# Kernel tuning notes

Measured on AMD Instinct MI355X. Metric: run time of the kernel, lower is better.

## Reference

```python
import jax, jax.numpy as jnp
import numpy as np

B, N, D = 32, 1024, 128


def setup_inputs() -> dict:
    key = jax.random.key(0)
    ks = jax.random.split(key, 8)
    scale = 0.05
    P = jax.random.normal(ks[0], (B, N, D), dtype=jnp.float32)
    w_itr_att = jax.random.normal(ks[1], (3 * D,), dtype=jnp.float32) * scale
    w1 = jax.random.normal(ks[2], (2 * D, D), dtype=jnp.float32) * scale
    w2 = jax.random.normal(ks[3], (2 * D, D), dtype=jnp.float32) * scale
    w3 = jax.random.normal(ks[4], (2 * D, D), dtype=jnp.float32) * scale
    b1 = jnp.zeros((D,), dtype=jnp.float32)
    b2 = jnp.zeros((D,), dtype=jnp.float32)
    b3 = jnp.zeros((D,), dtype=jnp.float32)
    return {"P": P, "w_itr_att": w_itr_att, "w1": w1, "w2": w2,
            "w3": w3, "b1": b1, "b2": b2, "b3": b3}


def reference(P, w_itr_att, w1, w2, w3, b1, b2, b3):
    # P: [b, n, d]
    d = P.shape[-1]
    # Original builds alphaP[b,i,:,j] = concat(P[b,j], P[b,i], P[b,j]*P[b,i])
    # and A[b,i,j] = w_itr_att . alphaP[b,i,:,j]. Decompose w to avoid the
    # O(n^2 * 3d) tensor while computing identical math.
    wa, wb, wc = w_itr_att[:d], w_itr_att[d:2 * d], w_itr_att[2 * d:]
    A = (P @ wb)[:, :, None] + (P @ wa)[:, None, :] \
        + jnp.einsum('bid,bjd->bij', P * wc, P)  # [b, n, n]
    SA = jax.nn.softmax(A, axis=-1)              # softmax over j (axis=2)
    itr_attn = jnp.einsum('bij,bjd->bid', SA, P)  # batch_dot(SA, P)
    # Fuse gate (dropout is identity at inference)
    P_concat = jnp.concatenate([P, itr_attn], axis=2)  # [b, n, 2d]
    z = jnp.tanh(P_concat @ w1 + b1)
    r = jax.nn.sigmoid(P_concat @ w2 + b2)
    f = jax.nn.sigmoid(P_concat @ w3 + b3)
    return r * P + f * z
```

## Files before the change

kernel.cpp:

```cpp
#include <hip/hip_runtime.h>
#include <math.h>

#define BB 32
#define NN 1024
#define DD 128

typedef __bf16 bf16;
typedef bf16 bf16x4 __attribute__((ext_vector_type(4)));
typedef bf16 bf16x8 __attribute__((ext_vector_type(8)));
typedef float f32x4 __attribute__((ext_vector_type(4)));
typedef float f32x16 __attribute__((ext_vector_type(16)));

#define MFMA16(a, b, c) __builtin_amdgcn_mfma_f32_16x16x32_bf16(a, b, c, 0, 0, 0)
#define MFMA32(a, b, c) __builtin_amdgcn_mfma_f32_32x32x16_bf16(a, b, c, 0, 0, 0)

__device__ inline bf16x4 swap32(bf16x4 v) {
    union { bf16x4 h; int i[2]; } u, r;
    u.h = v;
    r.i[0] = __shfl_xor(u.i[0], 32, 64);
    r.i[1] = __shfl_xor(u.i[1], 32, 64);
    return r.h;
}

#define LTS 133
__global__ __launch_bounds__(256) void k_prep(const float* __restrict__ P,
                                              const float* __restrict__ w_itr,
                                              bf16* __restrict__ Xbf,
                                              bf16* __restrict__ Pq,
                                              bf16* __restrict__ Ptp,
                                              float* __restrict__ t) {
    __shared__ float Lt[64 * LTS];
    int tid = threadIdx.x;
    int b = blockIdx.x >> 4, g = blockIdx.x & 15;
    int n0 = g * 64;
    long base = ((long)b * NN + n0) * DD;
#pragma unroll
    for (int i = 0; i < 8; ++i) {
        int idx = tid + i * 256;
        int row = idx >> 5, c4 = idx & 31;
        *(float4*)&Lt[row * LTS + c4 * 4] = *(const float4*)&P[base + row * 128 + c4 * 4];
    }
    __syncthreads();
    {
        int row = tid >> 2, q = tid & 3;
        float s = 0.f;
#pragma unroll
        for (int kk = 0; kk < 32; ++kk) {
            int k = 4 * kk + q;
            s += Lt[row * LTS + k] * w_itr[k];
        }
        s += __shfl_xor(s, 1);
        s += __shfl_xor(s, 2);
        if (q == 0) t[(long)b * NN + n0 + row] = s;
    }
    const float* wc = w_itr + 2 * DD;
#pragma unroll
    for (int i = 0; i < 4; ++i) {
        int idx = tid + i * 256;
        int row = idx >> 4, seg = idx & 15;
        float4 va = *(const float4*)&Lt[row * LTS + seg * 8];
        float4 vb = *(const float4*)&Lt[row * LTS + seg * 8 + 4];
        float4 wa4 = *(const float4*)&wc[seg * 8];
        float4 wb4 = *(const float4*)&wc[seg * 8 + 4];
        float fv[8] = {va.x, va.y, va.z, va.w, vb.x, vb.y, vb.z, vb.w};
        float wv[8] = {wa4.x, wa4.y, wa4.z, wa4.w, wb4.x, wb4.y, wb4.z, wb4.w};
        bf16x8 xv, qv;
#pragma unroll
        for (int e = 0; e < 8; ++e) {
            xv[e] = (bf16)fv[e];
            qv[e] = (bf16)(fv[e] * wv[e]);
        }
        long rowg = (long)b * NN + n0 + row;
        *(bf16x8*)&Xbf[rowg * 128 + seg * 8] = xv;
        *(bf16x8*)&Pq[rowg * 128 + seg * 8] = qv;
    }
#pragma unroll
    for (int i = 0; i < 4; ++i) {
        int idx = tid + i * 256;
        int d = idx >> 3, c = idx & 7;
        bf16x8 v;
#pragma unroll
        for (int e = 0; e < 8; ++e) v[e] = (bf16)Lt[(c * 8 + e) * LTS + d];
        *(bf16x8*)&Ptp[((long)b * DD + d) * NN + n0 + c * 8] = v;
    }
}

__global__ __launch_bounds__(256) void k_prepw(const float* __restrict__ w1,
                                               const float* __restrict__ w2,
                                               const float* __restrict__ w3,
                                               bf16* __restrict__ WtG) {
    __shared__ float Lw[32][33];
    int bi = blockIdx.x;
    int mat = bi >> 5, rem = bi & 31;
    int kt = rem >> 2, ct = rem & 3;
    const float* wsrc = (mat == 0) ? w1 : ((mat == 1) ? w2 : w3);
    int tid = threadIdx.x;
#pragma unroll
    for (int p = 0; p < 4; ++p) {
        int idx = tid + p * 256;
        int kr = idx >> 5, c = idx & 31;
        Lw[kr][c] = wsrc[(kt * 32 + kr) * DD + ct * 32 + c];
    }
    __syncthreads();
    int colg = tid >> 3, kq = tid & 7;
    bf16x4 v;
#pragma unroll
    for (int e = 0; e < 4; ++e) v[e] = (bf16)Lw[kq * 4 + e][colg];
    *(bf16x4*)&WtG[(mat * 128 + ct * 32 + colg) * 256 + kt * 32 + kq * 4] = v;
}

__global__ __launch_bounds__(256, 3) void k_attn(const bf16* __restrict__ Xbf,
                                                 const bf16* __restrict__ Pq,
                                                 const bf16* __restrict__ Ptp,
                                                 const float* __restrict__ t,
                                                 const bf16* __restrict__ WtG,
                                                 const float* __restrict__ b1,
                                                 const float* __restrict__ b2,
                                                 const float* __restrict__ b3,
                                                 float* __restrict__ out) {
    __shared__ __align__(16) char smem[51200];
    float* PA   = (float*)smem;
    bf16*  Wst  = (bf16*)smem;
    float* ost  = (float*)smem;
    bf16*  Xsh  = (bf16*)(smem + 33792);
    float* lbuf = (float*)(smem + 50688);

    const int tid = threadIdx.x;
    const int kh = tid >> 6, lane = tid & 63;
    const int col = lane & 31, q = lane >> 5;
    const int b = blockIdx.x & 31, qt = blockIdx.x >> 5;
    const long qrow0 = (long)b * NN + qt * 32;
    const long kvrow = (long)b * NN;

    bf16x8 Qb[8];
#pragma unroll
    for (int c = 0; c < 8; ++c)
        Qb[c] = *(const bf16x8*)&Pq[(qrow0 + col) * 128 + c * 16 + q * 8];

    f32x16 O[4];
#pragma unroll
    for (int mt = 0; mt < 4; ++mt)
#pragma unroll
        for (int r = 0; r < 16; ++r) O[mt][r] = 0.f;
    float lsum = 0.f;

    for (int kt = 0; kt < 8; ++kt) {
        int j0 = kh * 256 + kt * 32;
        bf16x8 kf[8];
#pragma unroll
        for (int c = 0; c < 8; ++c)
            kf[c] = *(const bf16x8*)&Xbf[(kvrow + j0 + col) * 128 + c * 16 + q * 8];
        bf16x8 vf[4][2];
#pragma unroll
        for (int mt = 0; mt < 4; ++mt)
#pragma unroll
            for (int kc = 0; kc < 2; ++kc)
                vf[mt][kc] = *(const bf16x8*)&Ptp[((long)b * DD + mt * 32 + col) * NN +
                                                  j0 + kc * 16 + q * 8];
        float tqs[16];
#pragma unroll
        for (int i = 0; i < 4; ++i) {
            float4 tv = *(const float4*)&t[kvrow + j0 + 8 * i + 4 * q];
            tqs[4 * i + 0] = tv.x; tqs[4 * i + 1] = tv.y;
            tqs[4 * i + 2] = tv.z; tqs[4 * i + 3] = tv.w;
        }
        f32x16 S;
#pragma unroll
        for (int r = 0; r < 16; ++r) S[r] = 0.f;
#pragma unroll
        for (int c = 0; c < 8; ++c) S = MFMA32(kf[c], Qb[c], S);

        float pv[16];
#pragma unroll
        for (int r = 0; r < 16; ++r) {
            float e = __expf(fminf(S[r] + tqs[r], 80.f));
            pv[r] = e;
            lsum += e;
        }
        bf16x4 Qd[4];
#pragma unroll
        for (int i = 0; i < 4; ++i)
#pragma unroll
            for (int e = 0; e < 4; ++e) Qd[i][e] = (bf16)pv[4 * i + e];
        bf16x4 sA = q ? Qd[0] : Qd[1];
        bf16x4 rA = swap32(sA);
        bf16x4 sB = q ? Qd[2] : Qd[3];
        bf16x4 rB = swap32(sB);
        bf16x4 lo0 = q ? rA : Qd[0], hi0 = q ? Qd[1] : rA;
        bf16x4 lo1 = q ? rB : Qd[2], hi1 = q ? Qd[3] : rB;
        bf16x8 f0, f1;
#pragma unroll
        for (int e = 0; e < 4; ++e) {
            f0[e] = lo0[e]; f0[4 + e] = hi0[e];
            f1[e] = lo1[e]; f1[4 + e] = hi1[e];
        }
#pragma unroll
        for (int mt = 0; mt < 4; ++mt) {
            O[mt] = MFMA32(vf[mt][0], f0, O[mt]);
            O[mt] = MFMA32(vf[mt][1], f1, O[mt]);
        }
    }

    float l2 = lsum + __shfl_xor(lsum, 32, 64);
    if (q == 0) lbuf[kh * 32 + col] = l2;
    if (kh & 1) {
        int slot = kh >> 1;
#pragma unroll
        for (int mt = 0; mt < 4; ++mt)
#pragma unroll
            for (int r = 0; r < 16; ++r) {
                int d = mt * 32 + (r & 3) + 8 * (r >> 2) + 4 * q;
                PA[slot * 4224 + d * 33 + col] = O[mt][r];
            }
    }
    __syncthreads();
    if (!(kh & 1)) {
        int slot = kh >> 1;
#pragma unroll
        for (int mt = 0; mt < 4; ++mt)
#pragma unroll
            for (int r = 0; r < 16; ++r) {
                int d = mt * 32 + (r & 3) + 8 * (r >> 2) + 4 * q;
                O[mt][r] += PA[slot * 4224 + d * 33 + col];
            }
    }
    __syncthreads();
    if (kh == 2) {
#pragma unroll
        for (int mt = 0; mt < 4; ++mt)
#pragma unroll
            for (int r = 0; r < 16; ++r) {
                int d = mt * 32 + (r & 3) + 8 * (r >> 2) + 4 * q;
                PA[d * 33 + col] = O[mt][r];
            }
    } else if (kh & 1) {
        int t128 = (kh >> 1) * 64 + lane;
#pragma unroll
        for (int i = 0; i < 4; ++i) {
            int idx = t128 + i * 128;
            int row = idx >> 4, seg = idx & 15;
            *(bf16x8*)&Xsh[row * 264 + seg * 8] =
                *(const bf16x8*)&Xbf[(qrow0 + row) * 128 + seg * 8];
        }
    }
    __syncthreads();
    if (kh == 0) {
        float ltot = lbuf[col] + lbuf[32 + col] + lbuf[64 + col] + lbuf[96 + col];
        float linv = 1.f / ltot;
#pragma unroll
        for (int mt = 0; mt < 4; ++mt)
#pragma unroll
            for (int r = 0; r < 16; ++r) {
                int d = mt * 32 + (r & 3) + 8 * (r >> 2) + 4 * q;
                float v = (O[mt][r] + PA[d * 33 + col]) * linv;
                Xsh[col * 264 + 128 + d] = (bf16)v;
            }
    }

    const int ln = lane & 15, q3 = lane >> 4;
    const int rh = kh & 1, ch = kh >> 1;
    f32x4 gz[4], gr[4];
    float rres[16];
#pragma unroll
    for (int mat = 0; mat < 3; ++mat) {
        f32x4 acc[4];
#pragma unroll
        for (int nt = 0; nt < 4; ++nt) acc[nt] = (f32x4){0.f, 0.f, 0.f, 0.f};
#pragma unroll
        for (int k2 = 0; k2 < 4; ++k2) {
            __syncthreads();
#pragma unroll
            for (int i = 0; i < 4; ++i) {
                int idx = tid + i * 256;
                *(float4*)&Wst[(idx >> 3) * 72 + (idx & 7) * 8] =
                    *(const float4*)&WtG[(mat * 128 + (idx >> 3)) * 256 + k2 * 64 +
                                         (idx & 7) * 8];
            }
            __syncthreads();
#pragma unroll
            for (int kc2 = 0; kc2 < 2; ++kc2) {
                bf16x8 Af = *(const bf16x8*)&Xsh[(rh * 16 + ln) * 264 + k2 * 64 +
                                                 kc2 * 32 + q3 * 8];
#pragma unroll
                for (int nt = 0; nt < 4; ++nt) {
                    bf16x8 Bf = *(const bf16x8*)&Wst[(ch * 64 + nt * 16 + ln) * 72 +
                                                     kc2 * 32 + q3 * 8];
                    acc[nt] = MFMA16(Af, Bf, acc[nt]);
                }
            }
        }
        const float* bp = (mat == 0) ? b1 : ((mat == 1) ? b2 : b3);
#pragma unroll
        for (int nt = 0; nt < 4; ++nt) {
            int colc = ch * 64 + nt * 16 + ln;
            float bb = bp[colc];
#pragma unroll
            for (int r = 0; r < 4; ++r) {
                float y = acc[nt][r] + bb;
                if (mat == 0) gz[nt][r] = tanhf(y);
                else if (mat == 1) gr[nt][r] = 1.f / (1.f + __expf(-y));
                else {
                    float fg = 1.f / (1.f + __expf(-y));
                    int lrow = rh * 16 + q3 * 4 + r;
                    float p = (float)Xsh[lrow * 264 + colc];
                    rres[nt * 4 + r] = gr[nt][r] * p + fg * gz[nt][r];
                }
            }
        }
    }
    __syncthreads();
#pragma unroll
    for (int nt = 0; nt < 4; ++nt)
#pragma unroll
        for (int r = 0; r < 4; ++r)
            ost[(rh * 16 + q3 * 4 + r) * 132 + ch * 64 + nt * 16 + ln] = rres[nt * 4 + r];
    __syncthreads();
#pragma unroll
    for (int i = 0; i < 4; ++i) {
        int idx = tid + i * 256;
        int row = idx >> 5, c4 = idx & 31;
        float4 v = *(const float4*)&ost[row * 132 + c4 * 4];
        *(float4*)&out[(qrow0 + row) * 128 + c4 * 4] = v;
    }
}

extern "C" void kernel_launch(void* const* d_in, const int* in_sizes, int n_in,
                              void* d_out, int out_size, void* d_ws, size_t ws_size,
                              hipStream_t stream) {
    const float* P     = (const float*)d_in[0];
    const float* w_itr = (const float*)d_in[1];
    const float* w1    = (const float*)d_in[2];
    const float* w2    = (const float*)d_in[3];
    const float* w3    = (const float*)d_in[4];
    const float* b1    = (const float*)d_in[5];
    const float* b2    = (const float*)d_in[6];
    const float* b3    = (const float*)d_in[7];
    float* out = (float*)d_out;

    char* wsb = (char*)d_ws;
    bf16* Xbf  = (bf16*)(wsb);
    bf16* Pq   = (bf16*)(wsb + 8388608);
    bf16* Ptp  = (bf16*)(wsb + 16777216);
    float* tws = (float*)(wsb + 25165824);
    bf16* WtG  = (bf16*)(wsb + 25296896);

    k_prep<<<dim3(BB * 16), dim3(256), 0, stream>>>(P, w_itr, Xbf, Pq, Ptp, tws);
    k_prepw<<<dim3(96), dim3(256), 0, stream>>>(w1, w2, w3, WtG);
    k_attn<<<dim3(1024), dim3(256), 0, stream>>>(Xbf, Pq, Ptp, tws, WtG, b1, b2, b3, out);
}
```

Baseline: 176.6 us.

## Switch attention to 16x16 MFMA with 2x2 query/key-split waves, merge prep kernels

The attention loop now uses 16x16x32 MFMAs. Each wave owns 16 query rows and half of the keys, replacing 32x32 tiles split four ways over keys. This shrinks the cross-wave reduction from four partial O tiles to two, cuts LDS use so more blocks fit, and drops the exp clamp. The weight-transpose kernel is folded into the prep kernel as extra blocks, and prep now uses 32-row tiles with register-based row loads, saving one launch. The trade-off is more shuffle work to rebuild the probability operand and twice the K/V fragment loads per query row, since each key tile is loaded by two waves.

```diff
diff --git a/kernel.cpp b/kernel.cpp
--- a/kernel.cpp
+++ b/kernel.cpp
@@ -9,104 +9,98 @@
 typedef bf16 bf16x4 __attribute__((ext_vector_type(4)));
 typedef bf16 bf16x8 __attribute__((ext_vector_type(8)));
 typedef float f32x4 __attribute__((ext_vector_type(4)));
-typedef float f32x16 __attribute__((ext_vector_type(16)));
 
 #define MFMA16(a, b, c) __builtin_amdgcn_mfma_f32_16x16x32_bf16(a, b, c, 0, 0, 0)
-#define MFMA32(a, b, c) __builtin_amdgcn_mfma_f32_32x32x16_bf16(a, b, c, 0, 0, 0)
-
-__device__ inline bf16x4 swap32(bf16x4 v) {
-    union { bf16x4 h; int i[2]; } u, r;
-    u.h = v;
-    r.i[0] = __shfl_xor(u.i[0], 32, 64);
-    r.i[1] = __shfl_xor(u.i[1], 32, 64);
-    return r.h;
-}
 
 #define LTS 133
 __global__ __launch_bounds__(256) void k_prep(const float* __restrict__ P,
                                               const float* __restrict__ w_itr,
+                                              const float* __restrict__ w1,
+                                              const float* __restrict__ w2,
+                                              const float* __restrict__ w3,
                                               bf16* __restrict__ Xbf,
                                               bf16* __restrict__ Pq,
                                               bf16* __restrict__ Ptp,
-                                              float* __restrict__ t) {
-    __shared__ float Lt[64 * LTS];
+                                              float* __restrict__ t,
+                                              bf16* __restrict__ WtG) {
+    __shared__ __align__(16) float Lt[32 * LTS];
     int tid = threadIdx.x;
-    int b = blockIdx.x >> 4, g = blockIdx.x & 15;
-    int n0 = g * 64;
-    long base = ((long)b * NN + n0) * DD;
-#pragma unroll
-    for (int i = 0; i < 8; ++i) {
+    if (blockIdx.x >= 1024) {
+        float (*Lw)[33] = (float(*)[33])Lt;
+        int bi = blockIdx.x - 1024;
+        int mat = bi >> 5, rem = bi & 31;
+        int kt = rem >> 2, ct = rem & 3;
+        const float* wsrc = (mat == 0) ? w1 : ((mat == 1) ? w2 : w3);
+#pragma unroll
+        for (int p = 0; p < 4; ++p) {
+            int idx = tid + p * 256;
+            Lw[idx >> 5][idx & 31] = wsrc[(kt * 32 + (idx >> 5)) * DD + ct * 32 + (idx & 31)];
+        }
+        __syncthreads();
+        int colg = tid >> 3, kq = tid & 7;
+        bf16x4 v;
+#pragma unroll
+        for (int e = 0; e < 4; ++e) v[e] = (bf16)Lw[kq * 4 + e][colg];
+        *(bf16x4*)&WtG[(mat * 128 + ct * 32 + colg) * 256 + kt * 32 + kq * 4] = v;
+        return;
+    }
+    int b = blockIdx.x >> 5, g = blockIdx.x & 31;
+    int n0 = g * 32;
+    int row = tid >> 3, q8 = tid & 7, d0 = q8 * 16;
+    long rowg = (long)b * NN + n0 + row;
+    float r[16];
+#pragma unroll
+    for (int i = 0; i < 4; ++i) {
+        float4 v = *(const float4*)&P[rowg * DD + d0 + 4 * i];
+        r[4 * i + 0] = v.x; r[4 * i + 1] = v.y; r[4 * i + 2] = v.z; r[4 * i + 3] = v.w;
+        *(float4*)&Lt[row * LTS + d0 + 4 * i] = v;
+    }
+    {
+        float wa[16];
+#pragma unroll
+        for (int i = 0; i < 4; ++i) {
+            float4 wv = *(const float4*)&w_itr[d0 + 4 * i];
+            wa[4 * i + 0] = wv.x; wa[4 * i + 1] = wv.y;
+            wa[4 * i + 2] = wv.z; wa[4 * i + 3] = wv.w;
+        }
+        float s = 0.f;
+#pragma unroll
+        for (int k = 0; k < 16; ++k) s += r[k] * wa[k];
+        s += __shfl_xor(s, 1); s += __shfl_xor(s, 2); s += __shfl_xor(s, 4);
+        if (q8 == 0) t[rowg] = s;
+    }
+    {
+        const float* wc = w_itr + 2 * DD;
+        float wcr[16];
+#pragma unroll
+        for (int i = 0; i < 4; ++i) {
+            float4 wv = *(const float4*)&wc[d0 + 4 * i];
+            wcr[4 * i + 0] = wv.x; wcr[4 * i + 1] = wv.y;
+            wcr[4 * i + 2] = wv.z; wcr[4 * i + 3] = wv.w;
+        }
+#pragma unroll
+        for (int h = 0; h < 2; ++h) {
+            bf16x8 xv, qv;
+#pragma unroll
+            for (int e = 0; e < 8; ++e) {
+                float f = r[8 * h + e];
+                xv[e] = (bf16)f;
+                qv[e] = (bf16)(f * wcr[8 * h + e]);
+            }
+            *(bf16x8*)&Xbf[rowg * DD + d0 + 8 * h] = xv;
+            *(bf16x8*)&Pq[rowg * DD + d0 + 8 * h] = qv;
+        }
+    }
+    __syncthreads();
+#pragma unroll
+    for (int i = 0; i < 2; ++i) {
         int idx = tid + i * 256;
-        int row = idx >> 5, c4 = idx & 31;
-        *(float4*)&Lt[row * LTS + c4 * 4] = *(const float4*)&P[base + row * 128 + c4 * 4];
-    }
-    __syncthreads();
-    {
-        int row = tid >> 2, q = tid & 3;
-        float s = 0.f;
-#pragma unroll
-        for (int kk = 0; kk < 32; ++kk) {
-            int k = 4 * kk + q;
-            s += Lt[row * LTS + k] * w_itr[k];
-        }
-        s += __shfl_xor(s, 1);
-        s += __shfl_xor(s, 2);
-        if (q == 0) t[(long)b * NN + n0 + row] = s;
-    }
-    const float* wc = w_itr + 2 * DD;
-#pragma unroll
-    for (int i = 0; i < 4; ++i) {
-        int idx = tid + i * 256;
-        int row = idx >> 4, seg = idx & 15;
-        float4 va = *(const float4*)&Lt[row * LTS + seg * 8];
-        float4 vb = *(const float4*)&Lt[row * LTS + seg * 8 + 4];
-        float4 wa4 = *(const float4*)&wc[seg * 8];
-        float4 wb4 = *(const float4*)&wc[seg * 8 + 4];
-        float fv[8] = {va.x, va.y, va.z, va.w, vb.x, vb.y, vb.z, vb.w};
-        float wv[8] = {wa4.x, wa4.y, wa4.z, wa4.w, wb4.x, wb4.y, wb4.z, wb4.w};
-        bf16x8 xv, qv;
-#pragma unroll
-        for (int e = 0; e < 8; ++e) {
-            xv[e] = (bf16)fv[e];
-            qv[e] = (bf16)(fv[e] * wv[e]);
-        }
-        long rowg = (long)b * NN + n0 + row;
-        *(bf16x8*)&Xbf[rowg * 128 + seg * 8] = xv;
-        *(bf16x8*)&Pq[rowg * 128 + seg * 8] = qv;
-    }
-#pragma unroll
-    for (int i = 0; i < 4; ++i) {
-        int idx = tid + i * 256;
-        int d = idx >> 3, c = idx & 7;
+        int d = idx >> 2, c = idx & 3;
         bf16x8 v;
 #pragma unroll
         for (int e = 0; e < 8; ++e) v[e] = (bf16)Lt[(c * 8 + e) * LTS + d];
         *(bf16x8*)&Ptp[((long)b * DD + d) * NN + n0 + c * 8] = v;
     }
-}
-
-__global__ __launch_bounds__(256) void k_prepw(const float* __restrict__ w1,
-                                               const float* __restrict__ w2,
-                                               const float* __restrict__ w3,
-                                               bf16* __restrict__ WtG) {
-    __shared__ float Lw[32][33];
-    int bi = blockIdx.x;
-    int mat = bi >> 5, rem = bi & 31;
-    int kt = rem >> 2, ct = rem & 3;
-    const float* wsrc = (mat == 0) ? w1 : ((mat == 1) ? w2 : w3);
-    int tid = threadIdx.x;
-#pragma unroll
-    for (int p = 0; p < 4; ++p) {
-        int idx = tid + p * 256;
-        int kr = idx >> 5, c = idx & 31;
-        Lw[kr][c] = wsrc[(kt * 32 + kr) * DD + ct * 32 + c];
-    }
-    __syncthreads();
-    int colg = tid >> 3, kq = tid & 7;
-    bf16x4 v;
-#pragma unroll
-    for (int e = 0; e < 4; ++e) v[e] = (bf16)Lw[kq * 4 + e][colg];
-    *(bf16x4*)&WtG[(mat * 128 + ct * 32 + colg) * 256 + kt * 32 + kq * 4] = v;
 }
 
 __global__ __launch_bounds__(256, 3) void k_attn(const bf16* __restrict__ Xbf,
@@ -118,147 +112,121 @@
                                                  const float* __restrict__ b2,
                                                  const float* __restrict__ b3,
                                                  float* __restrict__ out) {
-    __shared__ __align__(16) char smem[51200];
+    __shared__ __align__(16) char smem[35840];
     float* PA   = (float*)smem;
     bf16*  Wst  = (bf16*)smem;
     float* ost  = (float*)smem;
-    bf16*  Xsh  = (bf16*)(smem + 33792);
-    float* lbuf = (float*)(smem + 50688);
+    bf16*  Xsh  = (bf16*)(smem + 18432);
+    float* lbuf = (float*)(smem + 35328);
 
     const int tid = threadIdx.x;
-    const int kh = tid >> 6, lane = tid & 63;
-    const int col = lane & 31, q = lane >> 5;
+    const int w = tid >> 6, lane = tid & 63;
+    const int ln = lane & 15, qd = lane >> 4;
+    const int qsub = w & 1, kh = w >> 1;
     const int b = blockIdx.x & 31, qt = blockIdx.x >> 5;
     const long qrow0 = (long)b * NN + qt * 32;
     const long kvrow = (long)b * NN;
-
-    bf16x8 Qb[8];
-#pragma unroll
-    for (int c = 0; c < 8; ++c)
-        Qb[c] = *(const bf16x8*)&Pq[(qrow0 + col) * 128 + c * 16 + q * 8];
-
-    f32x16 O[4];
-#pragma unroll
-    for (int mt = 0; mt < 4; ++mt)
-#pragma unroll
-        for (int r = 0; r < 16; ++r) O[mt][r] = 0.f;
+    const long myq = qrow0 + qsub * 16;
+
+    bf16x8 Qb[4];
+#pragma unroll
+    for (int c = 0; c < 4; ++c)
+        Qb[c] = *(const bf16x8*)&Pq[(myq + ln) * DD + c * 32 + qd * 8];
+
+    f32x4 O[8];
+#pragma unroll
+    for (int dt = 0; dt < 8; ++dt) O[dt] = (f32x4){0.f, 0.f, 0.f, 0.f};
     float lsum = 0.f;
 
-    for (int kt = 0; kt < 8; ++kt) {
-        int j0 = kh * 256 + kt * 32;
-        bf16x8 kf[8];
-#pragma unroll
-        for (int c = 0; c < 8; ++c)
-            kf[c] = *(const bf16x8*)&Xbf[(kvrow + j0 + col) * 128 + c * 16 + q * 8];
-        bf16x8 vf[4][2];
-#pragma unroll
-        for (int mt = 0; mt < 4; ++mt)
-#pragma unroll
-            for (int kc = 0; kc < 2; ++kc)
-                vf[mt][kc] = *(const bf16x8*)&Ptp[((long)b * DD + mt * 32 + col) * NN +
-                                                  j0 + kc * 16 + q * 8];
-        float tqs[16];
+    for (int it = 0; it < 16; ++it) {
+        const int j0 = kh * 512 + it * 32;
+        bf16x8 kf0[4], kf1[4];
+#pragma unroll
+        for (int c = 0; c < 4; ++c) {
+            kf0[c] = *(const bf16x8*)&Xbf[(kvrow + j0 + ln) * DD + c * 32 + qd * 8];
+            kf1[c] = *(const bf16x8*)&Xbf[(kvrow + j0 + 16 + ln) * DD + c * 32 + qd * 8];
+        }
+        bf16x8 vf[8];
+#pragma unroll
+        for (int dt = 0; dt < 8; ++dt)
+            vf[dt] = *(const bf16x8*)&Ptp[((long)b * DD + dt * 16 + ln) * NN + j0 + qd * 8];
+        float4 tv0 = *(const float4*)&t[kvrow + j0 + 4 * qd];
+        float4 tv1 = *(const float4*)&t[kvrow + j0 + 16 + 4 * qd];
+
+        f32x4 S0 = (f32x4){0.f, 0.f, 0.f, 0.f}, S1 = S0;
+#pragma unroll
+        for (int c = 0; c < 4; ++c) S0 = MFMA16(kf0[c], Qb[c], S0);
+#pragma unroll
+        for (int c = 0; c < 4; ++c) S1 = MFMA16(kf1[c], Qb[c], S1);
+
+        float t0s[4] = {tv0.x, tv0.y, tv0.z, tv0.w};
+        float t1s[4] = {tv1.x, tv1.y, tv1.z, tv1.w};
+        bf16x4 a4, c4;
+#pragma unroll
+        for (int r = 0; r < 4; ++r) {
+            float e0 = __expf(S0[r] + t0s[r]);
+            float e1 = __expf(S1[r] + t1s[r]);
+            lsum += e0 + e1;
+            a4[r] = (bf16)e0;
+            c4[r] = (bf16)e1;
+        }
+        union { bf16x4 h; int i[2]; } ua, ub, s16, s32, s48, r16, r32, r48;
+        ua.h = a4; ub.h = c4;
+        s16.i[0] = (qd < 2) ? ua.i[0] : ub.i[0];
+        s16.i[1] = (qd < 2) ? ua.i[1] : ub.i[1];
+        r16.i[0] = __shfl_xor(s16.i[0], 16, 64);
+        r16.i[1] = __shfl_xor(s16.i[1], 16, 64);
+        s32.i[0] = (qd & 1) ? ua.i[0] : ub.i[0];
+        s32.i[1] = (qd & 1) ? ua.i[1] : ub.i[1];
+        r32.i[0] = __shfl_xor(s32.i[0], 32, 64);
+        r32.i[1] = __shfl_xor(s32.i[1], 32, 64);
+        s48.i[0] = (qd == 2) ? ua.i[0] : ub.i[0];
+        s48.i[1] = (qd == 2) ? ua.i[1] : ub.i[1];
+        r48.i[0] = __shfl_xor(s48.i[0], 48, 64);
+        r48.i[1] = __shfl_xor(s48.i[1], 48, 64);
+        union { bf16x8 h; int i[4]; } Bp;
+        int lo0 = (qd == 0) ? ua.i[0] : (qd == 1) ? r48.i[0] : (qd == 2) ? r32.i[0] : r16.i[0];
+        int lo1 = (qd == 0) ? ua.i[1] : (qd == 1) ? r48.i[1] : (qd == 2) ? r32.i[1] : r16.i[1];
+        int hi0 = (qd == 0) ? r16.i[0] : (qd == 1) ? r32.i[0] : (qd == 2) ? r48.i[0] : ub.i[0];
+        int hi1 = (qd == 0) ? r16.i[1] : (qd == 1) ? r32.i[1] : (qd == 2) ? r48.i[1] : ub.i[1];
+        Bp.i[0] = lo0; Bp.i[1] = lo1; Bp.i[2] = hi0; Bp.i[3] = hi1;
+#pragma unroll
+        for (int dt = 0; dt < 8; ++dt) O[dt] = MFMA16(vf[dt], Bp.h, O[dt]);
+    }
+
+    lsum += __shfl_xor(lsum, 16, 64);
+    lsum += __shfl_xor(lsum, 32, 64);
+    if (lane < 16) lbuf[kh * 32 + qsub * 16 + ln] = lsum;
+    if (kh == 1) {
+#pragma unroll
+        for (int dt = 0; dt < 8; ++dt)
+            *(f32x4*)&PA[(qsub * 16 + ln) * 132 + dt * 16 + qd * 4] = O[dt];
+    }
+    __syncthreads();
+    if (kh == 0) {
+        float ltot = lbuf[qsub * 16 + ln] + lbuf[32 + qsub * 16 + ln];
+        float linv = 1.f / ltot;
+#pragma unroll
+        for (int dt = 0; dt < 8; ++dt) {
+            f32x4 pa = *(const f32x4*)&PA[(qsub * 16 + ln) * 132 + dt * 16 + qd * 4];
+            bf16x4 o4;
+#pragma unroll
+            for (int r = 0; r < 4; ++r) o4[r] = (bf16)((O[dt][r] + pa[r]) * linv);
+            *(bf16x4*)&Xsh[(qsub * 16 + ln) * 264 + 128 + dt * 16 + qd * 4] = o4;
+        }
+    } else {
+        int tl = tid - 128;
 #pragma unroll
         for (int i = 0; i < 4; ++i) {
-            float4 tv = *(const float4*)&t[kvrow + j0 + 8 * i + 4 * q];
-            tqs[4 * i + 0] = tv.x; tqs[4 * i + 1] = tv.y;
-            tqs[4 * i + 2] = tv.z; tqs[4 * i + 3] = tv.w;
-        }
-        f32x16 S;
-#pragma unroll
-        for (int r = 0; r < 16; ++r) S[r] = 0.f;
-#pragma unroll
-        for (int c = 0; c < 8; ++c) S = MFMA32(kf[c], Qb[c], S);
-
-        float pv[16];
-#pragma unroll
-        for (int r = 0; r < 16; ++r) {
-            float e = __expf(fminf(S[r] + tqs[r], 80.f));
-            pv[r] = e;
-            lsum += e;
-        }
-        bf16x4 Qd[4];
-#pragma unroll
-        for (int i = 0; i < 4; ++i)
-#pragma unroll
-            for (int e = 0; e < 4; ++e) Qd[i][e] = (bf16)pv[4 * i + e];
-        bf16x4 sA = q ? Qd[0] : Qd[1];
-        bf16x4 rA = swap32(sA);
-        bf16x4 sB = q ? Qd[2] : Qd[3];
-        bf16x4 rB = swap32(sB);
-        bf16x4 lo0 = q ? rA : Qd[0], hi0 = q ? Qd[1] : rA;
-        bf16x4 lo1 = q ? rB : Qd[2], hi1 = q ? Qd[3] : rB;
-        bf16x8 f0, f1;
-#pragma unroll
-        for (int e = 0; e < 4; ++e) {
-            f0[e] = lo0[e]; f0[4 + e] = hi0[e];
-            f1[e] = lo1[e]; f1[4 + e] = hi1[e];
-        }
-#pragma unroll
-        for (int mt = 0; mt < 4; ++mt) {
-            O[mt] = MFMA32(vf[mt][0], f0, O[mt]);
-            O[mt] = MFMA32(vf[mt][1], f1, O[mt]);
-        }
-    }
-
-    float l2 = lsum + __shfl_xor(lsum, 32, 64);
-    if (q == 0) lbuf[kh * 32 + col] = l2;
-    if (kh & 1) {
-        int slot = kh >> 1;
-#pragma unroll
-        for (int mt = 0; mt < 4; ++mt)
-#pragma unroll
-            for (int r = 0; r < 16; ++r) {
-                int d = mt * 32 + (r & 3) + 8 * (r >> 2) + 4 * q;
-                PA[slot * 4224 + d * 33 + col] = O[mt][r];
-            }
-    }
-    __syncthreads();
-    if (!(kh & 1)) {
-        int slot = kh >> 1;
-#pragma unroll
-        for (int mt = 0; mt < 4; ++mt)
-#pragma unroll
-            for (int r = 0; r < 16; ++r) {
-                int d = mt * 32 + (r & 3) + 8 * (r >> 2) + 4 * q;
-                O[mt][r] += PA[slot * 4224 + d * 33 + col];
-            }
-    }
-    __syncthreads();
-    if (kh == 2) {
-#pragma unroll
-        for (int mt = 0; mt < 4; ++mt)
-#pragma unroll
-            for (int r = 0; r < 16; ++r) {
-                int d = mt * 32 + (r & 3) + 8 * (r >> 2) + 4 * q;
-                PA[d * 33 + col] = O[mt][r];
-            }
-    } else if (kh & 1) {
-        int t128 = (kh >> 1) * 64 + lane;
-#pragma unroll
-        for (int i = 0; i < 4; ++i) {
-            int idx = t128 + i * 128;
+            int idx = tl + i * 128;
             int row = idx >> 4, seg = idx & 15;
             *(bf16x8*)&Xsh[row * 264 + seg * 8] =
-                *(const bf16x8*)&Xbf[(qrow0 + row) * 128 + seg * 8];
-        }
-    }
-    __syncthreads();
-    if (kh == 0) {
-        float ltot = lbuf[col] + lbuf[32 + col] + lbuf[64 + col] + lbuf[96 + col];
-        float linv = 1.f / ltot;
-#pragma unroll
-        for (int mt = 0; mt < 4; ++mt)
-#pragma unroll
-            for (int r = 0; r < 16; ++r) {
-                int d = mt * 32 + (r & 3) + 8 * (r >> 2) + 4 * q;
-                float v = (O[mt][r] + PA[d * 33 + col]) * linv;
-                Xsh[col * 264 + 128 + d] = (bf16)v;
-            }
-    }
-
-    const int ln = lane & 15, q3 = lane >> 4;
-    const int rh = kh & 1, ch = kh >> 1;
+                *(const bf16x8*)&Xbf[(qrow0 + row) * DD + seg * 8];
+        }
+    }
+
+    const int q3 = lane >> 4;
+    const int rh = w & 1, ch = w >> 1;
     f32x4 gz[4], gr[4];
     float rres[16];
 #pragma unroll
@@ -318,9 +286,9 @@
 #pragma unroll
     for (int i = 0; i < 4; ++i) {
         int idx = tid + i * 256;
-        int row = idx >> 5, c4 = idx & 31;
-        float4 v = *(const float4*)&ost[row * 132 + c4 * 4];
-        *(float4*)&out[(qrow0 + row) * 128 + c4 * 4] = v;
+        int row = idx >> 5, c4i = idx & 31;
+        float4 v = *(const float4*)&ost[row * 132 + c4i * 4];
+        *(float4*)&out[(qrow0 + row) * DD + c4i * 4] = v;
     }
 }
 
@@ -344,7 +312,8 @@
     float* tws = (float*)(wsb + 25165824);
     bf16* WtG  = (bf16*)(wsb + 25296896);
 
-    k_prep<<<dim3(BB * 16), dim3(256), 0, stream>>>(P, w_itr, Xbf, Pq, Ptp, tws);
-    k_prepw<<<dim3(96), dim3(256), 0, stream>>>(w1, w2, w3, WtG);
-    k_attn<<<dim3(1024), dim3(256), 0, stream>>>(Xbf, Pq, Ptp, tws, WtG, b1, b2, b3, out);
+    k_prep<<<dim3(1120), dim3(256), 0, stream>>>(P, w_itr, w1, w2, w3,
+                                                 Xbf, Pq, Ptp, tws, WtG);
+    k_attn<<<dim3(1024), dim3(256), 0, stream>>>(Xbf, Pq, Ptp, tws, WtG,
+                                                 b1, b2, b3, out);
 }
```

New measurement: 221.0 us. +25.2%, slower.
